# Kernel optimization log

Measured on AMD Instinct MI355X. Metric: run time of the kernel, lower is better.

The kernel has to match this reference:

```python
import jax, jax.numpy as jnp
import numpy as np

B, L, D, H, NL = 2, 2048, 1024, 8, 2
HD = D // H
EPS = 1e-8


def layernorm(x, g, b):
    m = jnp.mean(x, axis=-1, keepdims=True)
    v = jnp.mean((x - m) ** 2, axis=-1, keepdims=True)
    return (x - m) / jnp.sqrt(v + EPS) * g + b


def rope(x):
    # x: [B, H, L, HD]; interleaved even/odd rotation as in the torch module
    Ls, Dh = x.shape[-2], x.shape[-1]
    pos = jnp.arange(Ls, dtype=jnp.float32)
    freqs = 1.0 / (10000.0 ** (jnp.arange(0, Dh, 2, dtype=jnp.float32) / Dh))
    ang = pos[:, None] * freqs[None, :]  # [L, HD/2]
    sin, cos = jnp.sin(ang), jnp.cos(ang)
    x1, x2 = x[..., ::2], x[..., 1::2]
    r1 = x1 * cos - x2 * sin
    r2 = x1 * sin + x2 * cos
    return jnp.stack([r1, r2], axis=-1).reshape(x.shape)


def setup_inputs() -> dict:
    key = jax.random.key(0)
    ks = jax.random.split(key, 16)
    s = 0.02

    def w(k, shape):
        return jax.random.normal(k, shape, dtype=jnp.float32) * s

    inp = {
        'seqs': jax.random.normal(ks[0], (B, L, D), dtype=jnp.float32),
        'attn_mask': jnp.broadcast_to(jnp.tril(jnp.ones((L, L), dtype=bool)), (B, L, L)),
        'Wq': w(ks[1], (NL, D, D)), 'bq': jnp.zeros((NL, D), jnp.float32),
        'Wk': w(ks[2], (NL, D, D)), 'bk': jnp.zeros((NL, D), jnp.float32),
        'Wu': w(ks[3], (NL, D, D)), 'bu': jnp.zeros((NL, D), jnp.float32),
        'Wv': w(ks[4], (NL, D, D)), 'bv': jnp.zeros((NL, D), jnp.float32),
        'Wo': w(ks[5], (NL, D, D)), 'bo': jnp.zeros((NL, D), jnp.float32),
        'W1': w(ks[6], (NL, D, D)), 'b1': jnp.zeros((NL, D), jnp.float32),
        'W2': w(ks[7], (NL, D, D)), 'b2': jnp.zeros((NL, D), jnp.float32),
        'ln1_g': jnp.ones((NL, D), jnp.float32), 'ln1_b': jnp.zeros((NL, D), jnp.float32),
        'ln2_g': jnp.ones((NL, D), jnp.float32), 'ln2_b': jnp.zeros((NL, D), jnp.float32),
        'lnf_g': jnp.ones((D,), jnp.float32), 'lnf_b': jnp.zeros((D,), jnp.float32),
    }
    return inp


def reference(seqs, attn_mask, Wq, bq, Wk, bk, Wu, bu, Wv, bv, Wo, bo,
              W1, b1, W2, b2, ln1_g, ln1_b, ln2_g, ln2_b, lnf_g, lnf_b):
    x = seqs
    Bsz, Ls, Dm = x.shape
    mask4 = attn_mask[:, None, :, :]  # [B,1,L,L]
    for i in range(NL):
        h = layernorm(x, ln1_g[i], ln1_b[i])

        def proj(Wm, bm):
            t = jnp.einsum('bld,od->blo', h, Wm) + bm
            return t.reshape(Bsz, Ls, H, HD).transpose(0, 2, 1, 3)

        Q = rope(proj(Wq[i], bq[i]))
        K = rope(proj(Wk[i], bk[i]))
        U = proj(Wu[i], bu[i])
        V = proj(Wv[i], bv[i])
        scores = jnp.einsum('bhqd,bhkd->bhqk', Q, K) / jnp.sqrt(jnp.float32(HD))
        scores = jnp.where(mask4, scores, jnp.float32(-1e9))
        wts = jax.nn.silu(scores)  # SiLU replaces softmax (HSTU)
        a = jnp.einsum('bhqk,bhkd->bhqd', wts, V) * U  # U-gated output
        a = a.transpose(0, 2, 1, 3).reshape(Bsz, Ls, Dm)
        a = jnp.einsum('bld,od->blo', a, Wo[i]) + bo[i]
        x = x + a
        h2 = layernorm(x, ln2_g[i], ln2_b[i])
        p = jnp.einsum('bld,od->blo', h2, W1[i]) + b1[i]
        f = jnp.einsum('bld,od->blo', p * jax.nn.silu(p), W2[i]) + b2[i]  # SwiGLU-style
        x = x + f
    return layernorm(x, lnf_g, lnf_b)
```

## Files before the change

kernel.cpp:

```cpp
#include <hip/hip_runtime.h>
#include <stdint.h>

typedef __attribute__((ext_vector_type(4))) float f32x4;
typedef __attribute__((ext_vector_type(16))) float f32x16;
typedef __attribute__((ext_vector_type(8))) short s16x8;
typedef __attribute__((ext_vector_type(4))) unsigned int u32x4;

#define D_ 1024
#define LQ 2048
#define HH_ 8
#define HD_ 128

static __device__ __forceinline__ float bf2f(ushort u){
  union { unsigned int i; float f; } v; v.i = ((unsigned int)u) << 16; return v.f;
}
static __device__ __forceinline__ ushort f2bf(float f){
  union { float f; unsigned int i; } v; v.f = f;
  unsigned int r = v.i + 0x7fffu + ((v.i >> 16) & 1u);
  return (ushort)(r >> 16);
}
static __device__ __forceinline__ unsigned int pkbf(float lo, float hi){
  unsigned int r;
  asm("v_cvt_pk_bf16_f32 %0, %1, %2" : "=v"(r) : "v"(lo), "v"(hi));
  return r;
}

struct WP { const float* s[7]; };
__global__ __launch_bounds__(256) void convert_weights(WP wp, ushort* __restrict__ dst){
  int w = blockIdx.x >> 7, blk = blockIdx.x & 127, t = threadIdx.x;
  const float4* s = (const float4*)wp.s[w];
  ushort4* d = (ushort4*)(dst + (size_t)w * 1048576);
  int base = blk * 2048 + t;
  #pragma unroll
  for (int r = 0; r < 8; r++){
    float4 v = s[base + r * 256];
    ushort4 o; o.x = f2bf(v.x); o.y = f2bf(v.y); o.z = f2bf(v.z); o.w = f2bf(v.w);
    d[base + r * 256] = o;
  }
}

template<int OUTF>
__global__ __launch_bounds__(256) void ln_kernel(const float* __restrict__ x,
    const float* __restrict__ g, const float* __restrict__ bb,
    float* __restrict__ outf, ushort* __restrict__ outb){
  int row = blockIdx.x, t = threadIdx.x;
  const float4* xr = (const float4*)(x + (size_t)row * D_);
  float4 v = xr[t];
  float s = v.x + v.y + v.z + v.w;
  float sq = v.x*v.x + v.y*v.y + v.z*v.z + v.w*v.w;
  #pragma unroll
  for (int o = 32; o; o >>= 1){ s += __shfl_down(s, o, 64); sq += __shfl_down(sq, o, 64); }
  __shared__ float red[8];
  int lane = t & 63, wv = t >> 6;
  if (!lane){ red[wv] = s; red[wv + 4] = sq; }
  __syncthreads();
  float S = red[0] + red[1] + red[2] + red[3];
  float SQ = red[4] + red[5] + red[6] + red[7];
  float m = S * (1.f / 1024.f);
  float var = SQ * (1.f / 1024.f) - m * m;
  float inv = rsqrtf(var + 1e-8f);
  float4 gv = ((const float4*)g)[t], bv = ((const float4*)bb)[t];
  float4 y;
  y.x = (v.x - m) * inv * gv.x + bv.x;
  y.y = (v.y - m) * inv * gv.y + bv.y;
  y.z = (v.z - m) * inv * gv.z + bv.z;
  y.w = (v.w - m) * inv * gv.w + bv.w;
  if (OUTF){
    ((float4*)outf)[(size_t)row * 256 + t] = y;
  } else {
    ushort4 o4; o4.x = f2bf(y.x); o4.y = f2bf(y.y); o4.z = f2bf(y.z); o4.w = f2bf(y.w);
    ((ushort4*)outb)[(size_t)row * 256 + t] = o4;
  }
}

struct P4 { ushort* d[4]; const float* b[4]; };

template<int EPI, int NB>
__global__ __launch_bounds__(256, 2) void gemm_k(
    const ushort* __restrict__ A, const ushort* __restrict__ W,
    P4 io, const float* __restrict__ resid, float* __restrict__ outf){
  __shared__ ushort As[128 * 64];
  __shared__ ushort Bs[128 * 64];
  int m0 = (blockIdx.x / NB) << 7;
  int n0 = (blockIdx.x % NB) << 7;
  int t = threadIdx.x, lane = t & 63, wv = t >> 6;
  int l15 = lane & 15, quad = lane >> 4;
  int wm = (wv & 1) << 6, wn = (wv >> 1) << 6;
  f32x4 acc[4][4] = {};
  for (int k0 = 0; k0 < 1024; k0 += 64){
    #pragma unroll
    for (int r = 0; r < 4; r++){
      int cb = r * 256 + wv * 64;
      int c = cb + lane;
      int row = c >> 3, j = c & 7;
      int kk = ((j ^ (row & 7)) << 3);
      __builtin_amdgcn_global_load_lds(
          (const __attribute__((address_space(1))) unsigned int*)(A + (size_t)(m0 + row) * 1024 + k0 + kk),
          (__attribute__((address_space(3))) unsigned int*)&As[cb * 8], 16, 0, 0);
      __builtin_amdgcn_global_load_lds(
          (const __attribute__((address_space(1))) unsigned int*)(W + (size_t)(n0 + row) * 1024 + k0 + kk),
          (__attribute__((address_space(3))) unsigned int*)&Bs[cb * 8], 16, 0, 0);
    }
    __syncthreads();
    #pragma unroll
    for (int kd = 0; kd < 2; kd++){
      s16x8 afr[4], bfr[4];
      #pragma unroll
      for (int mi = 0; mi < 4; mi++){
        int R = wm + mi * 16 + l15;
        afr[mi] = *(const s16x8*)&As[R * 64 + (((kd << 2) | quad) ^ (R & 7)) * 8];
      }
      #pragma unroll
      for (int ni = 0; ni < 4; ni++){
        int R = wn + ni * 16 + l15;
        bfr[ni] = *(const s16x8*)&Bs[R * 64 + (((kd << 2) | quad) ^ (R & 7)) * 8];
      }
      #pragma unroll
      for (int mi = 0; mi < 4; mi++)
        #pragma unroll
        for (int ni = 0; ni < 4; ni++)
          acc[mi][ni] = __builtin_amdgcn_mfma_f32_16x16x32_bf16(afr[mi], bfr[ni], acc[mi][ni], 0, 0, 0);
    }
    __syncthreads();
  }
  int sel = (EPI == 3) ? (n0 >> 10) : 0;
  ushort* dst = io.d[sel];
  const float* bias = io.b[sel];
  int ncol = (EPI == 3) ? (n0 & 1023) : n0;
  #pragma unroll
  for (int mi = 0; mi < 4; mi++){
    int gm = m0 + wm + mi * 16 + quad * 4;
    #pragma unroll
    for (int ni = 0; ni < 4; ni++){
      int cn = ncol + wn + ni * 16 + l15;
      float bv = bias[cn];
      if (EPI == 3 && sel < 2){
        int i2 = (cn & 127) >> 1;
        float freq = __builtin_amdgcn_exp2f(-0.20762050f * (float)i2);
        int odd = cn & 1;
        #pragma unroll
        for (int r = 0; r < 4; r++){
          float val = acc[mi][ni][r] + bv;
          float pv = __shfl_xor(val, 1, 64);
          int pos = (gm + r) & 2047;
          float ang = (float)pos * freq;
          float sv, cv; __sincosf(ang, &sv, &cv);
          float res = odd ? (pv * sv + val * cv) : (val * cv - pv * sv);
          dst[(size_t)(gm + r) * 1024 + cn] = f2bf(res);
        }
      } else {
        #pragma unroll
        for (int r = 0; r < 4; r++){
          float val = acc[mi][ni][r] + bv;
          size_t o = (size_t)(gm + r) * 1024 + cn;
          if (EPI == 1){ outf[o] = resid[o] + val; }
          else if (EPI == 2){
            float sg = __builtin_amdgcn_rcpf(1.f + __expf(-val));
            dst[o] = f2bf(val * val * sg);
          }
          else { dst[o] = f2bf(val); }
        }
      }
    }
  }
}

template<int EPI>
__global__ __launch_bounds__(256, 2) void gemm_k2(
    const ushort* __restrict__ A, const ushort* __restrict__ W,
    const float* __restrict__ bias, ushort* __restrict__ dst,
    const float* __restrict__ resid, float* __restrict__ outf){
  __shared__ ushort As[64 * 64];
  __shared__ ushort Bs[128 * 64];
  int m0 = (blockIdx.x >> 3) << 6;
  int n0 = (blockIdx.x & 7) << 7;
  int t = threadIdx.x, lane = t & 63, wv = t >> 6;
  int l15 = lane & 15, quad = lane >> 4;
  int wm = (wv & 1) << 5, wn = (wv >> 1) << 6;
  f32x4 acc[2][4] = {};
  for (int k0 = 0; k0 < 1024; k0 += 64){
    #pragma unroll
    for (int r = 0; r < 6; r++){
      int cb = (r < 2 ? r * 256 : (r - 2) * 256) + wv * 64;
      int c = cb + lane;
      int row = c >> 3, j = c & 7;
      int kk = ((j ^ (row & 7)) << 3);
      if (r < 2){
        __builtin_amdgcn_global_load_lds(
            (const __attribute__((address_space(1))) unsigned int*)(A + (size_t)(m0 + row) * 1024 + k0 + kk),
            (__attribute__((address_space(3))) unsigned int*)&As[cb * 8], 16, 0, 0);
      } else {
        __builtin_amdgcn_global_load_lds(
            (const __attribute__((address_space(1))) unsigned int*)(W + (size_t)(n0 + row) * 1024 + k0 + kk),
            (__attribute__((address_space(3))) unsigned int*)&Bs[cb * 8], 16, 0, 0);
      }
    }
    __syncthreads();
    #pragma unroll
    for (int kd = 0; kd < 2; kd++){
      s16x8 afr[2], bfr[4];
      #pragma unroll
      for (int mi = 0; mi < 2; mi++){
        int R = wm + mi * 16 + l15;
        afr[mi] = *(const s16x8*)&As[R * 64 + (((kd << 2) | quad) ^ (R & 7)) * 8];
      }
      #pragma unroll
      for (int ni = 0; ni < 4; ni++){
        int R = wn + ni * 16 + l15;
        bfr[ni] = *(const s16x8*)&Bs[R * 64 + (((kd << 2) | quad) ^ (R & 7)) * 8];
      }
      #pragma unroll
      for (int mi = 0; mi < 2; mi++)
        #pragma unroll
        for (int ni = 0; ni < 4; ni++)
          acc[mi][ni] = __builtin_amdgcn_mfma_f32_16x16x32_bf16(afr[mi], bfr[ni], acc[mi][ni], 0, 0, 0);
    }
    __syncthreads();
  }
  #pragma unroll
  for (int mi = 0; mi < 2; mi++){
    int gm = m0 + wm + mi * 16 + quad * 4;
    #pragma unroll
    for (int ni = 0; ni < 4; ni++){
      int cn = n0 + wn + ni * 16 + l15;
      float bv = bias[cn];
      #pragma unroll
      for (int r = 0; r < 4; r++){
        float val = acc[mi][ni][r] + bv;
        size_t o = (size_t)(gm + r) * 1024 + cn;
        if (EPI == 1){ outf[o] = resid[o] + val; }
        else {
          float sg = __builtin_amdgcn_rcpf(1.f + __expf(-val));
          dst[o] = f2bf(val * val * sg);
        }
      }
    }
  }
}

__global__ __launch_bounds__(256) void transpose_v(const ushort* __restrict__ Vb, ushort* __restrict__ Vt){
  int bidx = blockIdx.x;
  int dt = bidx & 1, lt = (bidx >> 1) & 31, bh = bidx >> 6;
  int b = bh >> 3, hh = bh & 7;
  int l0 = lt << 6, d0 = dt << 6;
  __shared__ ushort tile[64][66];
  int t = threadIdx.x;
  #pragma unroll
  for (int r = 0; r < 8; r++){
    int idx = r * 256 + t;
    int row = idx >> 5, cu = idx & 31;
    unsigned int val = *(const unsigned int*)(Vb + (size_t)(b * LQ + l0 + row) * D_ + hh * HD_ + d0 + cu * 2);
    *(unsigned int*)&tile[row][cu * 2] = val;
  }
  __syncthreads();
  #pragma unroll
  for (int r = 0; r < 8; r++){
    int idx = r * 256 + t;
    int drow = idx >> 5, lu = idx & 31;
    unsigned int val = (unsigned int)tile[lu * 2][drow] | ((unsigned int)tile[lu * 2 + 1][drow] << 16);
    int kk = lu * 2;
    int x = kk & 15;
    int kkp = (kk & 48) | ((x & 4) << 1) | ((x & 8) >> 1) | (x & 3);
    *(unsigned int*)(Vt + ((size_t)(bh * HD_ + d0 + drow)) * LQ + l0 + kkp) = val;
  }
}

__global__ __launch_bounds__(256, 2) void attn_kernel(
    const ushort* __restrict__ Q, const ushort* __restrict__ K,
    const ushort* __restrict__ Vt,
    ushort* __restrict__ Po0, ushort* __restrict__ Po1){
  __shared__ ushort Ks[2][64 * 128];
  __shared__ ushort Vs[2][128 * 64];
  int t = threadIdx.x, lane = t & 63, wv = t >> 6;
  int l31 = lane & 31, h = lane >> 5;
  int idx = blockIdx.x;
  int bh = idx & 15;
  int s = idx >> 4;
  int qt = (s < 16) ? (15 - (s >> 1)) : ((s - 16) >> 1);
  int half = s & 1;
  int ntiles = 2 * qt + 2;
  int c0 = qt + 1;
  int klo = half ? c0 : 0;
  int khi = half ? ntiles : c0;
  if (klo >= khi) return;
  int b = bh >> 3, hh = bh & 7;
  int q0 = qt << 7;
  const float scale = 0.08838834764831845f;

  s16x8 qf[8];
  const ushort* qbase = Q + (size_t)(b * LQ + q0 + (wv << 5) + l31) * D_ + hh * HD_;
  #pragma unroll
  for (int kd = 0; kd < 8; kd++) qf[kd] = *(const s16x8*)(qbase + kd * 16 + h * 8);

  auto STAGE = [&](int p, int kt){
    int k0 = kt << 6;
    #pragma unroll
    for (int r = 0; r < 4; r++){
      int cb = r * 256 + (wv << 6);
      int c = cb + lane;
      int R = c >> 4, sl = c & 15;
      int gg = sl ^ (R & 7);
      __builtin_amdgcn_global_load_lds(
          (const __attribute__((address_space(1))) unsigned int*)(K + (size_t)(b * LQ + k0 + R) * D_ + hh * HD_ + gg * 8),
          (__attribute__((address_space(3))) unsigned int*)&Ks[p][cb * 8], 16, 0, 0);
    }
    #pragma unroll
    for (int r = 0; r < 4; r++){
      int cb = r * 256 + (wv << 6);
      int c = cb + lane;
      int R = c >> 3, sl = c & 7;
      int gg = sl ^ (R & 7);
      __builtin_amdgcn_global_load_lds(
          (const __attribute__((address_space(1))) unsigned int*)(Vt + (size_t)(bh * HD_ + R) * LQ + k0 + gg * 8),
          (__attribute__((address_space(3))) unsigned int*)&Vs[p][cb * 8], 16, 0, 0);
    }
  };

  f32x16 acc_o[4] = {};
  int qg = q0 + (wv << 5) + l31;

  STAGE(0, klo);
  __syncthreads();
  for (int kt = klo; kt < khi; kt++){
    int p = (kt - klo) & 1;
    if (kt + 1 < khi) STAGE(p ^ 1, kt + 1);
    f32x16 sacc[2] = {};
    #pragma unroll
    for (int kd = 0; kd < 8; kd++){
      #pragma unroll
      for (int kb = 0; kb < 2; kb++){
        int R = (kb << 5) + l31;
        s16x8 af = *(const s16x8*)&Ks[p][(R * 16 + (((kd << 1) | h) ^ (R & 7))) * 8];
        sacc[kb] = __builtin_amdgcn_mfma_f32_32x32x16_bf16(af, qf[kd], sacc[kb], 0, 0, 0);
      }
    }
    int k0 = kt << 6;
    s16x8 pf[4];
    #pragma unroll
    for (int kb = 0; kb < 2; kb++){
      float pvv[16];
      #pragma unroll
      for (int r = 0; r < 16; r++){
        int kg = k0 + (kb << 5) + (r & 3) + ((r >> 2) << 3) + (h << 2);
        float sv = sacc[kb][r] * scale;
        float pp = sv * __builtin_amdgcn_rcpf(1.f + __expf(-sv));
        pvv[r] = (kg <= qg) ? pp : 0.f;
      }
      #pragma unroll
      for (int cc = 0; cc < 2; cc++){
        union { u32x4 u; s16x8 v; } w;
        w.u[0] = pkbf(pvv[cc*8+0], pvv[cc*8+1]);
        w.u[1] = pkbf(pvv[cc*8+2], pvv[cc*8+3]);
        w.u[2] = pkbf(pvv[cc*8+4], pvv[cc*8+5]);
        w.u[3] = pkbf(pvv[cc*8+6], pvv[cc*8+7]);
        pf[(kb << 1) | cc] = w.v;
      }
    }
    #pragma unroll
    for (int kv = 0; kv < 4; kv++){
      #pragma unroll
      for (int nt = 0; nt < 4; nt++){
        int R = (nt << 5) + l31;
        s16x8 vf = *(const s16x8*)&Vs[p][(R * 8 + (((kv << 1) | h) ^ (R & 7))) * 8];
        acc_o[nt] = __builtin_amdgcn_mfma_f32_32x32x16_bf16(pf[kv], vf, acc_o[nt], 0, 0, 0);
      }
    }
    __syncthreads();
  }
  ushort* Po = half ? Po1 : Po0;
  #pragma unroll
  for (int nt = 0; nt < 4; nt++){
    #pragma unroll
    for (int r = 0; r < 16; r++){
      int qq = q0 + (wv << 5) + (r & 3) + ((r >> 2) << 3) + (h << 2);
      int dd = (nt << 5) + l31;
      Po[(size_t)(b * LQ + qq) * D_ + hh * HD_ + dd] = f2bf(acc_o[nt][r]);
    }
  }
}

__global__ __launch_bounds__(256) void attn_reduce(
    const ushort* __restrict__ Po0, const ushort* __restrict__ Po1,
    const ushort* __restrict__ U, ushort* __restrict__ Aout){
  int i = (blockIdx.x * 256 + threadIdx.x) * 4;
  ushort4 p0 = *(const ushort4*)(Po0 + i);
  ushort4 p1 = *(const ushort4*)(Po1 + i);
  float v0 = bf2f(p0.x) + bf2f(p1.x);
  float v1 = bf2f(p0.y) + bf2f(p1.y);
  float v2 = bf2f(p0.z) + bf2f(p1.z);
  float v3 = bf2f(p0.w) + bf2f(p1.w);
  ushort4 u = *(const ushort4*)(U + i);
  ushort4 o;
  o.x = f2bf(v0 * bf2f(u.x)); o.y = f2bf(v1 * bf2f(u.y));
  o.z = f2bf(v2 * bf2f(u.z)); o.w = f2bf(v3 * bf2f(u.w));
  *(ushort4*)(Aout + i) = o;
}

extern "C" void kernel_launch(void* const* d_in, const int* in_sizes, int n_in,
                              void* d_out, int out_size, void* d_ws, size_t ws_size,
                              hipStream_t stream){
  const float* seqs = (const float*)d_in[0];
  const float* bq = (const float*)d_in[3];
  const float* bk = (const float*)d_in[5];
  const float* bu = (const float*)d_in[7];
  const float* bv = (const float*)d_in[9];
  const float* bo = (const float*)d_in[11];
  const float* b1 = (const float*)d_in[13];
  const float* b2 = (const float*)d_in[15];
  const float* ln1g = (const float*)d_in[16];
  const float* ln1b = (const float*)d_in[17];
  const float* ln2g = (const float*)d_in[18];
  const float* ln2b = (const float*)d_in[19];
  const float* lnfg = (const float*)d_in[20];
  const float* lnfb = (const float*)d_in[21];

  char* base = (char*)d_ws;
  const size_t MB = 1u << 20;
  if (ws_size < 78 * MB) return;
  ushort* wbf = (ushort*)base;
  ushort* h   = (ushort*)(base + 14 * MB);
  ushort* Qb  = (ushort*)(base + 22 * MB);
  ushort* Kb  = (ushort*)(base + 30 * MB);
  ushort* Ub  = (ushort*)(base + 38 * MB);
  ushort* Vb  = (ushort*)(base + 46 * MB);
  ushort* Vt  = (ushort*)(base + 54 * MB);
  float*  xb  = (float*)(base + 62 * MB);
  ushort* ab  = h;

  const size_t DD = 1048576;
  for (int i = 0; i < 2; i++){
    WP wp;
    for (int j = 0; j < 7; j++)
      wp.s[j] = (const float*)d_in[2 + 2 * j] + (size_t)i * DD;
    convert_weights<<<7 * 128, 256, 0, stream>>>(wp, wbf);
    const ushort* Wl = wbf;
    const float* xin = (i == 0) ? seqs : xb;
    ln_kernel<0><<<4096, 256, 0, stream>>>(xin, ln1g + i * D_, ln1b + i * D_, nullptr, h);
    P4 io_qkuv = {{Qb, Kb, Ub, Vb}, {bq + i * D_, bk + i * D_, bu + i * D_, bv + i * D_}};
    gemm_k<3, 32><<<1024, 256, 0, stream>>>(h, Wl, io_qkuv, nullptr, nullptr);
    transpose_v<<<1024, 256, 0, stream>>>(Vb, Vt);
    attn_kernel<<<512, 256, 0, stream>>>(Qb, Kb, Vt, ab, Vb);
    attn_reduce<<<4096, 256, 0, stream>>>(ab, Vb, Ub, ab);
    gemm_k2<1><<<512, 256, 0, stream>>>(ab, Wl + 4 * DD, bo + i * D_, nullptr, xin, xb);
    ln_kernel<0><<<4096, 256, 0, stream>>>(xb, ln2g + i * D_, ln2b + i * D_, nullptr, h);
    gemm_k2<2><<<512, 256, 0, stream>>>(h, Wl + 5 * DD, b1 + i * D_, Qb, nullptr, nullptr);
    gemm_k2<1><<<512, 256, 0, stream>>>(Qb, Wl + 6 * DD, b2 + i * D_, nullptr, xb, xb);
  }
  ln_kernel<1><<<4096, 256, 0, stream>>>(xb, lnfg, lnfb, (float*)d_out, nullptr);
}
```

Measured before the change: 485.8 us.

## Rewrite QKUV GEMM with 256x128 tiles and triple-buffered async LDS pipeline

The fused Q/K/U/V projection GEMM now uses 512-thread blocks with 256x128 output tiles and a three-stage LDS ring filled by global_load_lds. Loads run two k-tiles ahead, gated by s_waitcnt vmcnt and one barrier per iteration instead of two syncthreads. It also remaps block indices so neighbouring blocks share weight tiles, and raises wave priority around the MFMA bursts. The aim is to hide global-load latency and improve A/B reuse, at the cost of much more LDS per block (about 144 KB), which may limit occupancy.

```diff
diff --git a/kernel.cpp b/kernel.cpp
--- a/kernel.cpp
+++ b/kernel.cpp
@@ -75,66 +75,112 @@
 
 struct P4 { ushort* d[4]; const float* b[4]; };
 
-template<int EPI, int NB>
-__global__ __launch_bounds__(256, 2) void gemm_k(
-    const ushort* __restrict__ A, const ushort* __restrict__ W,
-    P4 io, const float* __restrict__ resid, float* __restrict__ outf){
-  __shared__ ushort As[128 * 64];
-  __shared__ ushort Bs[128 * 64];
-  int m0 = (blockIdx.x / NB) << 7;
-  int n0 = (blockIdx.x % NB) << 7;
+__global__ __launch_bounds__(512, 2) void gemm_qkuv(
+    const ushort* __restrict__ A, const ushort* __restrict__ W, P4 io){
+  __shared__ ushort As[3][256 * 64];
+  __shared__ ushort Bs[3][128 * 64];
+  int bid = (blockIdx.x & 7) * 64 + (blockIdx.x >> 3);
+  int m0 = (bid >> 5) << 8;
+  int n0g = (bid & 31) << 7;
   int t = threadIdx.x, lane = t & 63, wv = t >> 6;
   int l15 = lane & 15, quad = lane >> 4;
-  int wm = (wv & 1) << 6, wn = (wv >> 1) << 6;
-  f32x4 acc[4][4] = {};
-  for (int k0 = 0; k0 < 1024; k0 += 64){
+  int wm4 = (wv & 3) << 6;
+  int wn2 = (wv >> 2) << 6;
+
+  auto STAGE = [&](int buf, int kt){
+    int k0 = kt << 6;
     #pragma unroll
     for (int r = 0; r < 4; r++){
-      int cb = r * 256 + wv * 64;
-      int c = cb + lane;
-      int row = c >> 3, j = c & 7;
-      int kk = ((j ^ (row & 7)) << 3);
+      int g = r * 512 + (wv << 6);
+      int gl = g + lane;
+      int row = gl >> 3;
+      int kk = ((gl & 7) ^ (row & 7)) << 3;
       __builtin_amdgcn_global_load_lds(
           (const __attribute__((address_space(1))) unsigned int*)(A + (size_t)(m0 + row) * 1024 + k0 + kk),
-          (__attribute__((address_space(3))) unsigned int*)&As[cb * 8], 16, 0, 0);
+          (__attribute__((address_space(3))) unsigned int*)&As[buf][g * 8], 16, 0, 0);
+    }
+    #pragma unroll
+    for (int r = 0; r < 2; r++){
+      int g = r * 512 + (wv << 6);
+      int gl = g + lane;
+      int row = gl >> 3;
+      int kk = ((gl & 7) ^ (row & 7)) << 3;
       __builtin_amdgcn_global_load_lds(
-          (const __attribute__((address_space(1))) unsigned int*)(W + (size_t)(n0 + row) * 1024 + k0 + kk),
-          (__attribute__((address_space(3))) unsigned int*)&Bs[cb * 8], 16, 0, 0);
-    }
-    __syncthreads();
-    #pragma unroll
-    for (int kd = 0; kd < 2; kd++){
-      s16x8 afr[4], bfr[4];
-      #pragma unroll
-      for (int mi = 0; mi < 4; mi++){
-        int R = wm + mi * 16 + l15;
-        afr[mi] = *(const s16x8*)&As[R * 64 + (((kd << 2) | quad) ^ (R & 7)) * 8];
-      }
-      #pragma unroll
-      for (int ni = 0; ni < 4; ni++){
-        int R = wn + ni * 16 + l15;
-        bfr[ni] = *(const s16x8*)&Bs[R * 64 + (((kd << 2) | quad) ^ (R & 7)) * 8];
-      }
+          (const __attribute__((address_space(1))) unsigned int*)(W + (size_t)(n0g + row) * 1024 + k0 + kk),
+          (__attribute__((address_space(3))) unsigned int*)&Bs[buf][g * 8], 16, 0, 0);
+    }
+  };
+
+  f32x4 acc[4][4] = {};
+  STAGE(0, 0);
+  STAGE(1, 1);
+  int bc = 0, bs = 2;
+  for (int kt = 0; kt < 16; kt++){
+    if (kt < 15) asm volatile("s_waitcnt vmcnt(6)" ::: "memory");
+    else         asm volatile("s_waitcnt vmcnt(0)" ::: "memory");
+    __builtin_amdgcn_s_barrier();
+    asm volatile("" ::: "memory");
+    __builtin_amdgcn_sched_barrier(0);
+    if (kt + 2 < 16) STAGE(bs, kt + 2);
+    const ushort* Ab = &As[bc][0];
+    const ushort* Bb = &Bs[bc][0];
+    s16x8 afr[4][2];
+    #pragma unroll
+    for (int mi = 0; mi < 4; mi++)
+      #pragma unroll
+      for (int kd = 0; kd < 2; kd++){
+        int R = wm4 + mi * 16 + l15;
+        afr[mi][kd] = *(const s16x8*)&Ab[R * 64 + (((kd << 2) | quad) ^ (R & 7)) * 8];
+      }
+    s16x8 bfr[2][2];
+    #pragma unroll
+    for (int ni = 0; ni < 2; ni++)
+      #pragma unroll
+      for (int kd = 0; kd < 2; kd++){
+        int R = wn2 + ni * 16 + l15;
+        bfr[ni][kd] = *(const s16x8*)&Bb[R * 64 + (((kd << 2) | quad) ^ (R & 7)) * 8];
+      }
+    __builtin_amdgcn_s_setprio(1);
+    #pragma unroll
+    for (int kd = 0; kd < 2; kd++)
       #pragma unroll
       for (int mi = 0; mi < 4; mi++)
         #pragma unroll
-        for (int ni = 0; ni < 4; ni++)
-          acc[mi][ni] = __builtin_amdgcn_mfma_f32_16x16x32_bf16(afr[mi], bfr[ni], acc[mi][ni], 0, 0, 0);
-    }
-    __syncthreads();
-  }
-  int sel = (EPI == 3) ? (n0 >> 10) : 0;
+        for (int ni = 0; ni < 2; ni++)
+          acc[mi][ni] = __builtin_amdgcn_mfma_f32_16x16x32_bf16(afr[mi][kd], bfr[ni][kd], acc[mi][ni], 0, 0, 0);
+    __builtin_amdgcn_s_setprio(0);
+    s16x8 bfr2[2][2];
+    #pragma unroll
+    for (int ni = 0; ni < 2; ni++)
+      #pragma unroll
+      for (int kd = 0; kd < 2; kd++){
+        int R = wn2 + (ni + 2) * 16 + l15;
+        bfr2[ni][kd] = *(const s16x8*)&Bb[R * 64 + (((kd << 2) | quad) ^ (R & 7)) * 8];
+      }
+    __builtin_amdgcn_s_setprio(1);
+    #pragma unroll
+    for (int kd = 0; kd < 2; kd++)
+      #pragma unroll
+      for (int mi = 0; mi < 4; mi++)
+        #pragma unroll
+        for (int ni = 0; ni < 2; ni++)
+          acc[mi][ni + 2] = __builtin_amdgcn_mfma_f32_16x16x32_bf16(afr[mi][kd], bfr2[ni][kd], acc[mi][ni + 2], 0, 0, 0);
+    __builtin_amdgcn_s_setprio(0);
+    bc = (bc == 2) ? 0 : bc + 1;
+    bs = (bs == 2) ? 0 : bs + 1;
+  }
+  int sel = n0g >> 10;
   ushort* dst = io.d[sel];
   const float* bias = io.b[sel];
-  int ncol = (EPI == 3) ? (n0 & 1023) : n0;
+  int ncol = n0g & 1023;
   #pragma unroll
   for (int mi = 0; mi < 4; mi++){
-    int gm = m0 + wm + mi * 16 + quad * 4;
+    int gm = m0 + wm4 + mi * 16 + quad * 4;
     #pragma unroll
     for (int ni = 0; ni < 4; ni++){
-      int cn = ncol + wn + ni * 16 + l15;
+      int cn = ncol + wn2 + ni * 16 + l15;
       float bv = bias[cn];
-      if (EPI == 3 && sel < 2){
+      if (sel < 2){
         int i2 = (cn & 127) >> 1;
         float freq = __builtin_amdgcn_exp2f(-0.20762050f * (float)i2);
         int odd = cn & 1;
@@ -152,13 +198,7 @@
         #pragma unroll
         for (int r = 0; r < 4; r++){
           float val = acc[mi][ni][r] + bv;
-          size_t o = (size_t)(gm + r) * 1024 + cn;
-          if (EPI == 1){ outf[o] = resid[o] + val; }
-          else if (EPI == 2){
-            float sg = __builtin_amdgcn_rcpf(1.f + __expf(-val));
-            dst[o] = f2bf(val * val * sg);
-          }
-          else { dst[o] = f2bf(val); }
+          dst[(size_t)(gm + r) * 1024 + cn] = f2bf(val);
         }
       }
     }
@@ -437,7 +477,7 @@
     const float* xin = (i == 0) ? seqs : xb;
     ln_kernel<0><<<4096, 256, 0, stream>>>(xin, ln1g + i * D_, ln1b + i * D_, nullptr, h);
     P4 io_qkuv = {{Qb, Kb, Ub, Vb}, {bq + i * D_, bk + i * D_, bu + i * D_, bv + i * D_}};
-    gemm_k<3, 32><<<1024, 256, 0, stream>>>(h, Wl, io_qkuv, nullptr, nullptr);
+    gemm_qkuv<<<512, 512, 0, stream>>>(h, Wl, io_qkuv);
     transpose_v<<<1024, 256, 0, stream>>>(Vb, Vt);
     attn_kernel<<<512, 256, 0, stream>>>(Qb, Kb, Vt, ab, Vb);
     attn_reduce<<<4096, 256, 0, stream>>>(ab, Vb, Ub, ab);
```

New measurement: 506.1 us. 1.04x slower.
